# Kernel tuning notes

Hardware: AMD Instinct MI355X
Metric: run time of the kernel (lower is better)

The kernel has to match this reference:

```python
import jax, jax.numpy as jnp
import numpy as np

H, DI, N, R, B, L, K = 1024, 2048, 16, 64, 1, 2048, 4


def setup_inputs() -> dict:
    key = jax.random.key(0)
    ks = jax.random.split(key, 12)
    s = 0.02
    x = jax.random.normal(ks[0], (B, L, H), dtype=jnp.float32)
    in_proj_w = jax.random.normal(ks[1], (2 * DI, H), dtype=jnp.float32) * s
    in_proj_b = jax.random.normal(ks[2], (2 * DI,), dtype=jnp.float32) * s
    conv_w = jax.random.normal(ks[3], (DI, 1, K), dtype=jnp.float32) * s
    conv_b = jax.random.normal(ks[4], (DI,), dtype=jnp.float32) * s
    x_proj_w = jax.random.normal(ks[5], (R + 2 * N, DI), dtype=jnp.float32) * s
    dt_init_std = R ** (-0.5)
    dt_proj_w = jax.random.uniform(ks[6], (DI, R), dtype=jnp.float32, minval=-dt_init_std, maxval=dt_init_std)
    dt = jnp.exp(jax.random.uniform(ks[7], (DI,), dtype=jnp.float32) * (np.log(0.1) - np.log(0.001)) + np.log(0.001))
    dt = jnp.clip(dt, 0.0001, None)
    dt_proj_b = dt + jnp.log(-jnp.expm1(-dt))
    A_log = jnp.log(jnp.broadcast_to(jnp.arange(1, N + 1, dtype=jnp.float32)[None, :], (DI, N)))
    D = jnp.ones((DI,), dtype=jnp.float32)
    out_proj_w = jax.random.normal(ks[8], (H, DI), dtype=jnp.float32) * s
    return {"x": x, "in_proj_w": in_proj_w, "in_proj_b": in_proj_b, "conv_w": conv_w,
            "conv_b": conv_b, "x_proj_w": x_proj_w, "dt_proj_w": dt_proj_w,
            "dt_proj_b": dt_proj_b, "A_log": A_log, "D": D, "out_proj_w": out_proj_w}


def _mamba_fwd(x, in_proj_w, in_proj_b, conv_w, conv_b, x_proj_w, dt_proj_w, dt_proj_b, A_log, D, out_proj_w):
    b, l, _ = x.shape
    x_and_res = x @ in_proj_w.T + in_proj_b               # [b, l, 2*DI]
    xc, res = jnp.split(x_and_res, 2, axis=-1)
    # causal depthwise conv1d (padding K-1 then truncate to l == left-pad only)
    xt = jnp.transpose(xc, (0, 2, 1))                     # [b, DI, l]
    conv = jax.lax.conv_general_dilated(
        xt, conv_w, window_strides=(1,), padding=[(K - 1, 0)],
        dimension_numbers=("NCH", "OIH", "NCH"), feature_group_count=DI)
    conv = conv + conv_b[None, :, None]
    xs = jnp.transpose(jax.nn.silu(conv), (0, 2, 1))      # [b, l, DI]
    # SSM
    A = -jnp.exp(A_log.astype(jnp.float32))               # [DI, N]
    x_dbl = xs @ x_proj_w.T                               # [b, l, R+2N]
    delta, Bm, Cm = jnp.split(x_dbl, [R, R + N], axis=-1)
    delta = jax.nn.softplus(delta @ dt_proj_w.T + dt_proj_b)   # [b, l, DI]
    deltaA = jnp.exp(delta[..., None] * A[None, None])         # [b, l, DI, N]
    deltaB_u = delta[..., None] * Bm[:, :, None, :] * xs[..., None]

    def comb(c1, c2):
        a1, u1 = c1
        a2, u2 = c2
        return a2 * a1, a2 * u1 + u2

    _, h = jax.lax.associative_scan(comb, (deltaA, deltaB_u), axis=1)
    y = jnp.einsum("bldn,bln->bld", h, Cm) + xs * D.astype(jnp.float32)
    y = y * jax.nn.silu(res)
    return y @ out_proj_w.T                               # [b, l, H]


def reference(x, in_proj_w, in_proj_b, conv_w, conv_b, x_proj_w, dt_proj_w, dt_proj_b, A_log, D, out_proj_w):
    return _mamba_fwd(x, in_proj_w, in_proj_b, conv_w, conv_b, x_proj_w,
                      dt_proj_w, dt_proj_b, A_log, D, out_proj_w)
```

## Files before the change

kernel.cpp:

```cpp
#include <hip/hip_runtime.h>
#include <hip/hip_bf16.h>
#include <math.h>

#define H_DIM 1024
#define DI    2048
#define NS    16
#define RR    64
#define LL    2048
#define NC    64
#define CL    32
#define KSPL  16

typedef __bf16 bf16x8 __attribute__((ext_vector_type(8)));
typedef __bf16 bf16x4 __attribute__((ext_vector_type(4)));
typedef float  f32x4  __attribute__((ext_vector_type(4)));

__device__ __forceinline__ float silu_f(float x)  { return x / (1.f + __expf(-x)); }
__device__ __forceinline__ float softplus_f(float x) {
    const float l = __logf(1.f + __expf(x));
    return x > 15.f ? x : l;
}

__device__ __forceinline__ void gload16(const void* g, void* l) {
    __builtin_amdgcn_global_load_lds(
        (const __attribute__((address_space(1))) void*)g,
        (__attribute__((address_space(3))) void*)l, 16, 0, 0);
}

__device__ __forceinline__ void f2b4(const float* __restrict__ in,
                                     __bf16* __restrict__ out)
{
    float4 v = *(const float4*)in;
    bf16x4 o;
    o[0] = (__bf16)v.x; o[1] = (__bf16)v.y; o[2] = (__bf16)v.z; o[3] = (__bf16)v.w;
    *(bf16x4*)out = o;
}

__device__ __forceinline__ void xcd_swz(int nx, int ny, int& bx, int& by)
{
    const int nwg = nx * ny;
    const int bid = by * nx + bx;
    const int cpx = nwg >> 3;
    const int s   = (bid & 7) * cpx + (bid >> 3);
    bx = s % nx;  by = s / nx;
}

#define SEG0 (LL * H_DIM)
#define SEG1 (2 * DI * H_DIM)
#define SEG2 (H_DIM * DI)
#define SEG3 (DI * RR)
#define SEG4 (128 * DI)
#define CUM0 SEG0
#define CUM1 (CUM0 + SEG1)
#define CUM2 (CUM1 + SEG2)
#define CUM3 (CUM2 + SEG3)
#define CUMT (CUM3 + SEG4)

__global__ __launch_bounds__(256) void convert_all_k(
    const float* __restrict__ x,    const float* __restrict__ in_w,
    const float* __restrict__ outw, const float* __restrict__ dtw,
    const float* __restrict__ xpw,
    __bf16* __restrict__ x_bf,    __bf16* __restrict__ inw_bf,
    __bf16* __restrict__ outw_bf, __bf16* __restrict__ dtw_bf,
    __bf16* __restrict__ xpw_pad)
{
    const int i = (blockIdx.x * 256 + threadIdx.x) * 4;
    if (i < CUM0) {
        f2b4(x + i, x_bf + i);
    } else if (i < CUM1) {
        const int o = i - CUM0;  f2b4(in_w + o, inw_bf + o);
    } else if (i < CUM2) {
        const int o = i - CUM1;  f2b4(outw + o, outw_bf + o);
    } else if (i < CUM3) {
        const int o = i - CUM2;  f2b4(dtw + o, dtw_bf + o);
    } else if (i < CUMT) {
        const int o = i - CUM3;
        const int row = o >> 11;
        if (row < 96) {
            f2b4(xpw + o, xpw_pad + o);
        } else {
            bf16x4 z; z[0] = z[1] = z[2] = z[3] = (__bf16)0.f;
            *(bf16x4*)&xpw_pad[o] = z;
        }
    }
}

__global__ __launch_bounds__(256) void reduce_xdbl_k(
    const float* __restrict__ part, float* __restrict__ xdbl,
    __bf16* __restrict__ xdbl_bf)
{
    const int idx = blockIdx.x * 256 + threadIdx.x;
    float s = 0.f;
    #pragma unroll
    for (int z = 0; z < KSPL; ++z) s += part[(size_t)z * (LL * 96) + idx];
    xdbl[idx] = s;
    xdbl_bf[idx] = (__bf16)s;
}

__global__ __launch_bounds__(256) void reduce_out_k(
    const float* __restrict__ part, float* __restrict__ out)
{
    const int i = (blockIdx.x * 256 + threadIdx.x) * 4;
    f32x4 a = *(const f32x4*)&part[i];
    f32x4 b = *(const f32x4*)&part[(size_t)LL * H_DIM + i];
    *(f32x4*)&out[i] = a + b;
}

__global__ __launch_bounds__(256) void gemm_inproj_k(
    const __bf16* __restrict__ A,
    const __bf16* __restrict__ W,
    const float* __restrict__ bias,
    __bf16* __restrict__ xc_bf,
    __bf16* __restrict__ res_bf)
{
    __shared__ __bf16 smA[2][64 * 32];
    __shared__ __bf16 smB[2][128 * 32];
    const int t    = threadIdx.x;
    const int lane = t & 63;
    int bx = blockIdx.x, by = blockIdx.y;
    xcd_swz(32, 32, bx, by);
    const int m0 = by * 64, n0 = bx * 128;
    const int wr = ((t >> 6) >> 1) * 32;
    const int wc = ((t >> 6) & 1) * 64;

    const int srow = t >> 2;
    const int skof = (t & 3) * 8;
    const int lds_base = (t >> 6) * 512;

    const int offA = (wr + (lane & 15)) * 32 + ((lane >> 4) * 8);
    const int offB = (wc + (lane & 15)) * 32 + ((lane >> 4) * 8);

    f32x4 acc[2][4] = {};

#define STAGE_IP(buf, k0)                                                          \
    do {                                                                           \
        gload16(A + (size_t)(m0 + srow)      * H_DIM + (k0) + skof, &smA[buf][lds_base]);        \
        gload16(W + (size_t)(n0 + srow)      * H_DIM + (k0) + skof, &smB[buf][lds_base]);        \
        gload16(W + (size_t)(n0 + 64 + srow) * H_DIM + (k0) + skof, &smB[buf][2048 + lds_base]); \
    } while (0)

    STAGE_IP(0, 0);
    __syncthreads();
    int cur = 0;
    for (int k0 = 0; k0 < H_DIM; k0 += 32) {
        if (k0 + 32 < H_DIM) STAGE_IP(cur ^ 1, k0 + 32);

        bf16x8 af[2], bfr[4];
        #pragma unroll
        for (int m = 0; m < 2; ++m) af[m]  = *(const bf16x8*)&smA[cur][offA + m * 512];
        #pragma unroll
        for (int n = 0; n < 4; ++n) bfr[n] = *(const bf16x8*)&smB[cur][offB + n * 512];
        #pragma unroll
        for (int m = 0; m < 2; ++m)
            #pragma unroll
            for (int n = 0; n < 4; ++n)
                acc[m][n] = __builtin_amdgcn_mfma_f32_16x16x32_bf16(
                    af[m], bfr[n], acc[m][n], 0, 0, 0);
        __syncthreads();
        cur ^= 1;
    }
#undef STAGE_IP

    __bf16* outp = (n0 < DI) ? xc_bf : res_bf;
    const int ncol0 = (n0 < DI) ? n0 : n0 - DI;
    const int rbase = m0 + wr + ((lane >> 4) << 2);
    const int cbase = ncol0 + wc + (lane & 15);
    #pragma unroll
    for (int n = 0; n < 4; ++n) {
        const int col = cbase + n * 16;
        const float bv = bias[(n0 < DI ? 0 : DI) + col];
        #pragma unroll
        for (int m = 0; m < 2; ++m)
            #pragma unroll
            for (int j = 0; j < 4; ++j)
                outp[(size_t)(rbase + m * 16 + j) * DI + col] =
                    (__bf16)(acc[m][n][j] + bv);
    }
}

template<int BIAS, int ACT, int SPLITK, int SWZ>
__global__ __launch_bounds__(256) void gemm64_bf16_nt(
    const __bf16* __restrict__ A, int lda,
    const __bf16* __restrict__ W, int ldw,
    const float* __restrict__ bias,
    float* __restrict__ C, int ldc, int ncols, size_t pstride,
    int K)
{
    __shared__ __bf16 smA[2][64 * 32];
    __shared__ __bf16 smB[2][128 * 32];
    const int t    = threadIdx.x;
    const int lane = t & 63;
    int bx = blockIdx.x, by = blockIdx.y;
    if (SWZ) xcd_swz(gridDim.x, gridDim.y, bx, by);
    const int m0 = by * 64, n0 = bx * 128;
    const int wr = ((t >> 6) >> 1) * 32;
    const int wc = ((t >> 6) & 1) * 64;

    const int srow = t >> 2;
    const int skof = (t & 3) * 8;
    const int lds_base = (t >> 6) * 512;

    const int offA = (wr + (lane & 15)) * 32 + ((lane >> 4) * 8);
    const int offB = (wc + (lane & 15)) * 32 + ((lane >> 4) * 8);

    const int kseg  = K / SPLITK;
    const int kbase = (SPLITK > 1) ? blockIdx.z * kseg : 0;
    const int kend  = kbase + kseg;

    f32x4 acc[2][4] = {};

#define STAGE_64(buf, k0)                                                          \
    do {                                                                           \
        gload16(A + (size_t)(m0 + srow)      * lda + (k0) + skof, &smA[buf][lds_base]);        \
        gload16(W + (size_t)(n0 + srow)      * ldw + (k0) + skof, &smB[buf][lds_base]);        \
        gload16(W + (size_t)(n0 + 64 + srow) * ldw + (k0) + skof, &smB[buf][2048 + lds_base]); \
    } while (0)

    STAGE_64(0, kbase);
    __syncthreads();
    int cur = 0;
    for (int k0 = kbase; k0 < kend; k0 += 32) {
        if (k0 + 32 < kend) STAGE_64(cur ^ 1, k0 + 32);

        bf16x8 af[2], bfr[4];
        #pragma unroll
        for (int m = 0; m < 2; ++m) af[m]  = *(const bf16x8*)&smA[cur][offA + m * 512];
        #pragma unroll
        for (int n = 0; n < 4; ++n) bfr[n] = *(const bf16x8*)&smB[cur][offB + n * 512];
        #pragma unroll
        for (int m = 0; m < 2; ++m)
            #pragma unroll
            for (int n = 0; n < 4; ++n)
                acc[m][n] = __builtin_amdgcn_mfma_f32_16x16x32_bf16(
                    af[m], bfr[n], acc[m][n], 0, 0, 0);
        __syncthreads();
        cur ^= 1;
    }
#undef STAGE_64

    float* Cp = C + ((SPLITK > 1) ? (size_t)blockIdx.z * pstride : 0);
    const int rbase = m0 + wr + ((lane >> 4) << 2);
    const int cbase = n0 + wc + (lane & 15);
    #pragma unroll
    for (int n = 0; n < 4; ++n) {
        const int col = cbase + n * 16;
        if (col >= ncols) continue;
        const float bv = BIAS ? bias[col] : 0.f;
        #pragma unroll
        for (int m = 0; m < 2; ++m) {
            #pragma unroll
            for (int j = 0; j < 4; ++j) {
                float v = acc[m][n][j] + bv;
                if (ACT == 1) v = softplus_f(v);
                Cp[(size_t)(rbase + m * 16 + j) * ldc + col] = v;
            }
        }
    }
}

__global__ __launch_bounds__(256) void conv_silu_k(
    const __bf16* __restrict__ xc, const float* __restrict__ cw,
    const float* __restrict__ cb, __bf16* __restrict__ xs_bf)
{
    const int idx = blockIdx.x * 256 + threadIdx.x;
    const int l  = idx >> 8;
    const int d0 = (idx & 255) * 8;

    float r0[8] = {}, r1[8] = {}, r2[8] = {}, r3[8];
    bf16x8 v;
    if (l >= 3) { v = *(const bf16x8*)&xc[(size_t)(l-3)*DI + d0];
                  #pragma unroll
                  for (int j = 0; j < 8; ++j) r0[j] = (float)v[j]; }
    if (l >= 2) { v = *(const bf16x8*)&xc[(size_t)(l-2)*DI + d0];
                  #pragma unroll
                  for (int j = 0; j < 8; ++j) r1[j] = (float)v[j]; }
    if (l >= 1) { v = *(const bf16x8*)&xc[(size_t)(l-1)*DI + d0];
                  #pragma unroll
                  for (int j = 0; j < 8; ++j) r2[j] = (float)v[j]; }
    v = *(const bf16x8*)&xc[(size_t)l*DI + d0];
    #pragma unroll
    for (int j = 0; j < 8; ++j) r3[j] = (float)v[j];

    bf16x8 o;
    #pragma unroll
    for (int j = 0; j < 8; ++j) {
        const int d = d0 + j;
        float4 w = *(const float4*)&cw[d * 4];
        float a = cb[d];
        a = fmaf(r0[j], w.x, a);
        a = fmaf(r1[j], w.y, a);
        a = fmaf(r2[j], w.z, a);
        a = fmaf(r3[j], w.w, a);
        o[j] = (__bf16)silu_f(a);
    }
    *(bf16x8*)&xs_bf[(size_t)l*DI + d0] = o;
}

__global__ __launch_bounds__(256) void scan1_k(
    const float* __restrict__ delta, const __bf16* __restrict__ xs,
    const float* __restrict__ A_log, const float* __restrict__ xdbl,
    float* __restrict__ P, float* __restrict__ S)
{
    const int d = blockIdx.x * 256 + threadIdx.x;
    const int c = blockIdx.y;
    float A[NS];
    #pragma unroll
    for (int n = 0; n < NS; ++n) A[n] = -__expf(A_log[d * NS + n]);
    float h[NS] = {};
    float ap[NS];
    #pragma unroll
    for (int n = 0; n < NS; ++n) ap[n] = 1.f;

    const int l0 = c * CL;
    for (int l = l0; l < l0 + CL; ++l) {
        const float dt = delta[(size_t)l * DI + d];
        const float u  = (float)xs[(size_t)l * DI + d];
        const float du = dt * u;
        #pragma unroll
        for (int n = 0; n < NS; ++n) {
            const float Bn = xdbl[(size_t)l * 96 + RR + n];
            const float dA = __expf(dt * A[n]);
            h[n]  = fmaf(dA, h[n], du * Bn);
            ap[n] *= dA;
        }
    }
    const size_t base = ((size_t)c * DI + d) * NS;
    #pragma unroll
    for (int n = 0; n < NS; ++n) { P[base + n] = ap[n]; S[base + n] = h[n]; }
}

__global__ __launch_bounds__(256) void scan2_k(
    const float* __restrict__ P, const float* __restrict__ S, float* __restrict__ Hp)
{
    const int idx = blockIdx.x * 256 + threadIdx.x;
    float h = 0.f;
    for (int c = 0; c < NC; ++c) {
        const size_t o = (size_t)c * DI * NS + idx;
        Hp[o] = h;
        h = fmaf(P[o], h, S[o]);
    }
}

__global__ __launch_bounds__(256) void scan3_k(
    const float* __restrict__ delta, const __bf16* __restrict__ xs,
    const float* __restrict__ A_log, const float* __restrict__ xdbl,
    const float* __restrict__ Hp, const __bf16* __restrict__ res_bf,
    const float* __restrict__ Dp, __bf16* __restrict__ y_bf)
{
    const int d = blockIdx.x * 256 + threadIdx.x;
    const int c = blockIdx.y;
    float A[NS];
    #pragma unroll
    for (int n = 0; n < NS; ++n) A[n] = -__expf(A_log[d * NS + n]);
    float h[NS];
    const size_t base = ((size_t)c * DI + d) * NS;
    #pragma unroll
    for (int n = 0; n < NS; ++n) h[n] = Hp[base + n];
    const float Dd = Dp[d];

    const int l0 = c * CL;
    for (int l = l0; l < l0 + CL; ++l) {
        const float dt = delta[(size_t)l * DI + d];
        const float u  = (float)xs[(size_t)l * DI + d];
        const float du = dt * u;
        float acc = 0.f;
        #pragma unroll
        for (int n = 0; n < NS; ++n) {
            const float Bn = xdbl[(size_t)l * 96 + RR + n];
            const float Cn = xdbl[(size_t)l * 96 + RR + NS + n];
            const float dA = __expf(dt * A[n]);
            h[n] = fmaf(dA, h[n], du * Bn);
            acc  = fmaf(h[n], Cn, acc);
        }
        float yv = fmaf(u, Dd, acc);
        const float r = (float)res_bf[(size_t)l * DI + d];
        yv *= silu_f(r);
        y_bf[(size_t)l * DI + d] = (__bf16)yv;
    }
}

extern "C" void kernel_launch(void* const* d_in, const int* in_sizes, int n_in,
                              void* d_out, int out_size, void* d_ws, size_t ws_size,
                              hipStream_t stream)
{
    const float* x        = (const float*)d_in[0];
    const float* in_w     = (const float*)d_in[1];
    const float* in_b     = (const float*)d_in[2];
    const float* conv_w   = (const float*)d_in[3];
    const float* conv_b   = (const float*)d_in[4];
    const float* xproj_w  = (const float*)d_in[5];
    const float* dtproj_w = (const float*)d_in[6];
    const float* dtproj_b = (const float*)d_in[7];
    const float* A_log    = (const float*)d_in[8];
    const float* Dp       = (const float*)d_in[9];
    const float* outw     = (const float*)d_in[10];
    float* out = (float*)d_out;

    float* ws    = (float*)d_ws;
    float* delta = ws;
    float* xdbl  = delta + (size_t)LL * DI;
    float* P     = xdbl  + (size_t)LL * 96;
    float* S     = P     + (size_t)NC * DI * NS;
    float* Hp    = S     + (size_t)NC * DI * NS;
    float* opart = Hp    + (size_t)NC * DI * NS;
    float* xpart = delta;
    __bf16* x_bf    = (__bf16*)(opart + (size_t)2 * LL * H_DIM);
    __bf16* inw_bf  = x_bf    + (size_t)LL * H_DIM;
    __bf16* outw_bf = inw_bf  + (size_t)2 * DI * H_DIM;
    __bf16* dtw_bf  = outw_bf + (size_t)H_DIM * DI;
    __bf16* xdbl_bf = dtw_bf  + (size_t)DI * RR;
    __bf16* y_bf    = xdbl_bf + (size_t)LL * 96;
    __bf16* xs_bf   = y_bf    + (size_t)LL * DI;
    __bf16* xc_bf   = xs_bf   + (size_t)LL * DI;
    __bf16* res_bf  = xc_bf   + (size_t)LL * DI;
    __bf16* xpw_pad = res_bf  + (size_t)LL * DI;

    const dim3 blk(256);

    convert_all_k<<<dim3(CUMT / 1024), blk, 0, stream>>>(
        x, in_w, outw, dtproj_w, xproj_w,
        x_bf, inw_bf, outw_bf, dtw_bf, xpw_pad);

    gemm_inproj_k<<<dim3((2*DI)/128, LL/64), blk, 0, stream>>>(
        x_bf, inw_bf, in_b, xc_bf, res_bf);

    conv_silu_k<<<dim3((LL*DI)/(8*256)), blk, 0, stream>>>(xc_bf, conv_w, conv_b, xs_bf);

    gemm64_bf16_nt<0,0,KSPL,0><<<dim3(1, LL/64, KSPL), blk, 0, stream>>>(
        xs_bf, DI, xpw_pad, DI, nullptr, xpart, 96, 96, (size_t)LL * 96, DI);
    reduce_xdbl_k<<<dim3((LL * 96) / 256), blk, 0, stream>>>(xpart, xdbl, xdbl_bf);

    gemm64_bf16_nt<1,1,1,1><<<dim3(DI/128, LL/64), blk, 0, stream>>>(
        xdbl_bf, 96, dtw_bf, RR, dtproj_b, delta, DI, DI, 0, RR);

    scan1_k<<<dim3(DI/256, NC), blk, 0, stream>>>(delta, xs_bf, A_log, xdbl, P, S);
    scan2_k<<<dim3((DI*NS)/256), blk, 0, stream>>>(P, S, Hp);
    scan3_k<<<dim3(DI/256, NC), blk, 0, stream>>>(delta, xs_bf, A_log, xdbl, Hp, res_bf, Dp, y_bf);

    gemm64_bf16_nt<0,0,2,1><<<dim3(H_DIM/128, LL/64, 2), blk, 0, stream>>>(
        y_bf, DI, outw_bf, DI, nullptr, opart, H_DIM, H_DIM, (size_t)LL * H_DIM, DI);
    reduce_out_k<<<dim3((LL * H_DIM) / 1024), blk, 0, stream>>>(opart, out);
}
```

Before: 242.6 us.

## Triple-buffer GEMM LDS tiles with vmcnt waits and a single barrier per step

Both bf16 GEMM kernels move from double to triple LDS buffering. Loads are issued two k-steps ahead, and the start of each step uses a partial s_waitcnt vmcnt(3) plus a raw s_barrier in place of two __syncthreads. The aim is to keep more global-to-LDS loads in flight and cut the barrier stalls in the k-loop. In exchange the kernels use more shared memory, which may lower occupancy. Correctness also depends on the exact count of outstanding vm operations, so the hand-written waitcnt values are fragile.

Measured after the change: 243.7 us. About the same (+0.4%).

```diff
diff --git a/kernel.cpp b/kernel.cpp
--- a/kernel.cpp
+++ b/kernel.cpp
@@ -106,6 +106,9 @@
     *(f32x4*)&out[i] = a + b;
 }
 
+#define WAIT_VM3()  asm volatile("s_waitcnt vmcnt(3)" ::: "memory")
+#define WAIT_VM0()  asm volatile("s_waitcnt vmcnt(0)" ::: "memory")
+
 __global__ __launch_bounds__(256) void gemm_inproj_k(
     const __bf16* __restrict__ A,
     const __bf16* __restrict__ W,
@@ -113,8 +116,8 @@
     __bf16* __restrict__ xc_bf,
     __bf16* __restrict__ res_bf)
 {
-    __shared__ __bf16 smA[2][64 * 32];
-    __shared__ __bf16 smB[2][128 * 32];
+    __shared__ __bf16 smA[3][64 * 32];
+    __shared__ __bf16 smB[3][128 * 32];
     const int t    = threadIdx.x;
     const int lane = t & 63;
     int bx = blockIdx.x, by = blockIdx.y;
@@ -139,25 +142,26 @@
         gload16(W + (size_t)(n0 + 64 + srow) * H_DIM + (k0) + skof, &smB[buf][2048 + lds_base]); \
     } while (0)
 
+    const int nk = H_DIM / 32;
     STAGE_IP(0, 0);
-    __syncthreads();
-    int cur = 0;
-    for (int k0 = 0; k0 < H_DIM; k0 += 32) {
-        if (k0 + 32 < H_DIM) STAGE_IP(cur ^ 1, k0 + 32);
+    STAGE_IP(1, 32);
+    for (int ks = 0; ks < nk; ++ks) {
+        if (ks + 1 < nk) WAIT_VM3(); else WAIT_VM0();
+        __builtin_amdgcn_s_barrier();
+        if (ks + 2 < nk) STAGE_IP((ks + 2) % 3, (ks + 2) * 32);
+        const int cb = ks % 3;
 
         bf16x8 af[2], bfr[4];
         #pragma unroll
-        for (int m = 0; m < 2; ++m) af[m]  = *(const bf16x8*)&smA[cur][offA + m * 512];
-        #pragma unroll
-        for (int n = 0; n < 4; ++n) bfr[n] = *(const bf16x8*)&smB[cur][offB + n * 512];
+        for (int m = 0; m < 2; ++m) af[m]  = *(const bf16x8*)&smA[cb][offA + m * 512];
+        #pragma unroll
+        for (int n = 0; n < 4; ++n) bfr[n] = *(const bf16x8*)&smB[cb][offB + n * 512];
         #pragma unroll
         for (int m = 0; m < 2; ++m)
             #pragma unroll
             for (int n = 0; n < 4; ++n)
                 acc[m][n] = __builtin_amdgcn_mfma_f32_16x16x32_bf16(
                     af[m], bfr[n], acc[m][n], 0, 0, 0);
-        __syncthreads();
-        cur ^= 1;
     }
 #undef STAGE_IP
 
@@ -186,8 +190,8 @@
     float* __restrict__ C, int ldc, int ncols, size_t pstride,
     int K)
 {
-    __shared__ __bf16 smA[2][64 * 32];
-    __shared__ __bf16 smB[2][128 * 32];
+    __shared__ __bf16 smA[3][64 * 32];
+    __shared__ __bf16 smB[3][128 * 32];
     const int t    = threadIdx.x;
     const int lane = t & 63;
     int bx = blockIdx.x, by = blockIdx.y;
@@ -205,7 +209,6 @@
 
     const int kseg  = K / SPLITK;
     const int kbase = (SPLITK > 1) ? blockIdx.z * kseg : 0;
-    const int kend  = kbase + kseg;
 
     f32x4 acc[2][4] = {};
 
@@ -216,25 +219,26 @@
         gload16(W + (size_t)(n0 + 64 + srow) * ldw + (k0) + skof, &smB[buf][2048 + lds_base]); \
     } while (0)
 
+    const int nk = kseg / 32;
     STAGE_64(0, kbase);
-    __syncthreads();
-    int cur = 0;
-    for (int k0 = kbase; k0 < kend; k0 += 32) {
-        if (k0 + 32 < kend) STAGE_64(cur ^ 1, k0 + 32);
+    if (nk > 1) STAGE_64(1, kbase + 32);
+    for (int ks = 0; ks < nk; ++ks) {
+        if (ks + 1 < nk) WAIT_VM3(); else WAIT_VM0();
+        __builtin_amdgcn_s_barrier();
+        if (ks + 2 < nk) STAGE_64((ks + 2) % 3, kbase + (ks + 2) * 32);
+        const int cb = ks % 3;
 
         bf16x8 af[2], bfr[4];
         #pragma unroll
-        for (int m = 0; m < 2; ++m) af[m]  = *(const bf16x8*)&smA[cur][offA + m * 512];
-        #pragma unroll
-        for (int n = 0; n < 4; ++n) bfr[n] = *(const bf16x8*)&smB[cur][offB + n * 512];
+        for (int m = 0; m < 2; ++m) af[m]  = *(const bf16x8*)&smA[cb][offA + m * 512];
+        #pragma unroll
+        for (int n = 0; n < 4; ++n) bfr[n] = *(const bf16x8*)&smB[cb][offB + n * 512];
         #pragma unroll
         for (int m = 0; m < 2; ++m)
             #pragma unroll
             for (int n = 0; n < 4; ++n)
                 acc[m][n] = __builtin_amdgcn_mfma_f32_16x16x32_bf16(
                     af[m], bfr[n], acc[m][n], 0, 0, 0);
-        __syncthreads();
-        cur ^= 1;
     }
 #undef STAGE_64
 
```
